# Optimization experiments

Hardware: AMD Instinct MI355X
Metric: run time of the kernel (lower is better)

Reference implementation:

```python
import jax, jax.numpy as jnp
import numpy as np

T, A, D = 1024, 512, 128
EPS = 1e-5
NEG_SLOPE = 0.01  # torch LeakyReLU default


def setup_inputs() -> dict:
    key = jax.random.key(0)
    ks = jax.random.split(key, 5)
    return {
        "nf_task": jax.random.normal(ks[0], (T, D), dtype=jnp.float32),
        "nf_agent": jax.random.normal(ks[1], (A, D), dtype=jnp.float32),
        "W1": jax.random.normal(ks[2], (D, 2 * D), dtype=jnp.float32) * 0.05,
        "gamma1": jnp.ones((D,), dtype=jnp.float32),
        "beta1": jnp.zeros((D,), dtype=jnp.float32),
        "W2": jax.random.normal(ks[3], (1, D), dtype=jnp.float32) * 0.05,
        "gamma2": jnp.ones((1,), dtype=jnp.float32),
        "beta2": jnp.zeros((1,), dtype=jnp.float32),
        "finished": jax.random.randint(ks[4], (T,), 0, 2, dtype=jnp.int32),
    }


def reference(nf_task, nf_agent, W1, gamma1, beta1, W2, gamma2, beta2, finished):
    d = nf_task.shape[1]
    # Linear(2D->D, no bias) on concat([src, dst]) == src @ W_src^T + dst @ W_dst^T
    src_proj = nf_task @ W1[:, :d].T   # [T, D]
    dst_proj = nf_agent @ W1[:, d:].T  # [A, D]
    h = src_proj[:, None, :] + dst_proj[None, :, :]  # per-edge hidden [T, A, D]
    # BatchNorm1d(D), training mode: batch stats over all edges
    mean = h.mean(axis=(0, 1))
    var = h.var(axis=(0, 1))  # biased, as torch uses for normalization
    h = (h - mean) * jax.lax.rsqrt(var + EPS) * gamma1 + beta1
    # LeakyReLU
    h = jnp.where(h >= 0, h, NEG_SLOPE * h)
    # Linear(D->1, no bias)
    s = jnp.einsum('tad,d->ta', h, W2[0])  # [T, A]
    # BatchNorm1d(1), training mode over all edges
    m2 = s.mean()
    v2 = s.var()
    s = (s - m2) * jax.lax.rsqrt(v2 + EPS) * gamma2[0] + beta2[0]
    # mask edges whose src task is finished
    s = jnp.where(finished.astype(bool)[:, None], -jnp.inf, s)
    # reduce: each agent's mailbox = scores over incoming tasks -> policy [A, T]
    return s.T
```

## Files before the change

### kernel.cpp

```cpp
#include <hip/hip_runtime.h>
#include <math.h>
#include <float.h>

#define T_N 1024
#define A_N 512
#define D_N 128
#define EPS 1e-5f
#define LDP 132

#define WS_SP   0
#define WS_DP   (WS_SP + T_N*D_N)
#define WS_SUMS (WS_DP + A_N*D_N)
#define WS_P    (WS_SUMS + 512)
#define WS_Q    (WS_P + T_N)
#define WS_S2   (WS_Q + A_N)
#define WS_ST   199168
#define N2F     ((float)(T_N * A_N))

__global__ __launch_bounds__(64) void k1_proj(const float* __restrict__ task,
                                              const float* __restrict__ agent,
                                              const float* __restrict__ W1,
                                              float* __restrict__ ws)
{
    __shared__ float RT[32 * LDP];
    __shared__ float WT[32 * LDP];
    int b = blockIdx.x;
    int rt = b >> 2, ct = b & 3;
    int tid = threadIdx.x;

    if (b == 0) {
        for (int i = 0; i < 8; i++) ws[WS_SUMS + tid + i * 64] = 0.f;
    }

    const float* src; float* dst; int woff, rbase;
    if (rt < 32) { src = task;  dst = ws + WS_SP; woff = 0;    rbase = rt * 32; }
    else         { src = agent; dst = ws + WS_DP; woff = D_N;  rbase = (rt - 32) * 32; }
    int cbase = ct * 32;

    {
        int rr = tid >> 5;
        int k  = (tid & 31) * 4;
        for (int it = 0; it < 16; it++) {
            int r = it * 2 + rr;
            *(float4*)(RT + r * LDP + k) = *(const float4*)(src + (rbase + r) * D_N + k);
        }
        for (int it = 0; it < 16; it++) {
            int j = it * 2 + rr;
            *(float4*)(WT + j * LDP + k) = *(const float4*)(W1 + (cbase + j) * (2 * D_N) + woff + k);
        }
    }
    __syncthreads();

    int rg = tid >> 3, cg = tid & 7;
    float acc[4][4] = {};
    for (int kk = 0; kk < 32; kk++) {
        float4 rv[4], wv[4];
        for (int i = 0; i < 4; i++) rv[i] = *(const float4*)(RT + (rg + 8 * i) * LDP + kk * 4);
        for (int j = 0; j < 4; j++) wv[j] = *(const float4*)(WT + (cg + 8 * j) * LDP + kk * 4);
        for (int i = 0; i < 4; i++)
            for (int j = 0; j < 4; j++)
                acc[i][j] += rv[i].x * wv[j].x + rv[i].y * wv[j].y
                           + rv[i].z * wv[j].z + rv[i].w * wv[j].w;
    }
    for (int i = 0; i < 4; i++)
        for (int j = 0; j < 4; j++)
            dst[(rbase + rg + 8 * i) * D_N + cbase + cg + 8 * j] = acc[i][j];
}

__global__ __launch_bounds__(256) void k2_stats(float* __restrict__ ws)
{
    int b = blockIdx.x, tid = threadIdx.x;
    int j = tid & 127, rh = tid >> 7;
    const float* src; float* sums; int rbase;
    if (b < 32) { src = ws + WS_SP; sums = ws + WS_SUMS;       rbase = b * 32; }
    else        { src = ws + WS_DP; sums = ws + WS_SUMS + 256; rbase = (b - 32) * 32; }
    float s = 0.f, q = 0.f;
    for (int i = 0; i < 16; i++) {
        float v = src[(rbase + i * 2 + rh) * D_N + j];
        s += v; q += v * v;
    }
    atomicAdd(&sums[j], s);
    atomicAdd(&sums[j + 128], q);
}

__global__ __launch_bounds__(64) void k2b_scale_pq(const float* __restrict__ g1,
                                                   const float* __restrict__ b1,
                                                   const float* __restrict__ W2,
                                                   float* __restrict__ ws)
{
    __shared__ float sc[128], sh[128], wl[128];
    int b = blockIdx.x, tid = threadIdx.x;
    if (b == 0 && tid < 2) ws[WS_S2 + tid] = 0.f;

    for (int h = 0; h < 2; h++) {
        int j = tid + 64 * h;
        float ms = ws[WS_SUMS + j]       * (1.f / T_N);
        float vs = ws[WS_SUMS + 128 + j] * (1.f / T_N) - ms * ms;
        float md = ws[WS_SUMS + 256 + j] * (1.f / A_N);
        float vd = ws[WS_SUMS + 384 + j] * (1.f / A_N) - md * md;
        float mean = ms + md, var = vs + vd;
        float s = g1[j] / sqrtf(var + EPS);
        sc[j] = s;
        sh[j] = b1[j] - mean * s;
        wl[j] = W2[j];
    }
    __syncthreads();

    float* rows; float* PQ; int rbase; bool isdp;
    if (b < 128) { rows = ws + WS_SP; PQ = ws + WS_P; rbase = b * 8;         isdp = false; }
    else         { rows = ws + WS_DP; PQ = ws + WS_Q; rbase = (b - 128) * 8; isdp = true;  }

    int l = tid;
    for (int r = 0; r < 8; r++) {
        int row = rbase + r;
        float v0 = rows[row * D_N + l];
        float v1 = rows[row * D_N + 64 + l];
        v0 = v0 * sc[l]      + (isdp ? sh[l]      : 0.f);
        v1 = v1 * sc[l + 64] + (isdp ? sh[l + 64] : 0.f);
        rows[row * D_N + l]      = v0;
        rows[row * D_N + 64 + l] = v1;
        float p = v0 * wl[l] + v1 * wl[l + 64];
        for (int off = 32; off >= 1; off >>= 1) p += __shfl_xor(p, off);
        if (l == 0) PQ[row] = 0.505f * p;
    }
}

#define TT 64
#define TA 32
__global__ __launch_bounds__(256) void kd_main(const float* __restrict__ W2,
                                               float* __restrict__ ws)
{
    __shared__ float spT[TT * LDP];
    __shared__ float dpT[TA * LDP];
    __shared__ float w495[128];
    __shared__ float Pl[TT], Ql[TA];
    __shared__ float stile[TA * 68];
    __shared__ float red[512];

    int tid = threadIdx.x;
    int rowbase = blockIdx.x * TT;
    int colbase = blockIdx.y * TA;

    {
        int k  = (tid & 31) * 4;
        int r8 = tid >> 5;
        for (int it = 0; it < 8; it++) {
            int t = it * 8 + r8;
            *(float4*)(spT + t * LDP + k) = *(const float4*)(ws + WS_SP + (rowbase + t) * D_N + k);
        }
        for (int it = 0; it < 4; it++) {
            int a = it * 8 + r8;
            *(float4*)(dpT + a * LDP + k) = *(const float4*)(ws + WS_DP + (colbase + a) * D_N + k);
        }
    }
    if (tid < 128) w495[tid] = 0.495f * W2[tid];
    if (tid < TT)  Pl[tid] = ws[WS_P + rowbase + tid];
    if (tid >= 128 && tid < 128 + TA) Ql[tid - 128] = ws[WS_Q + colbase + (tid - 128)];
    __syncthreads();

    int tx = tid & 15, ty = tid >> 4;
    float acc[4][2] = {};
    for (int kk = 0; kk < 32; kk++) {
        float4 wv = *(const float4*)(w495 + kk * 4);
        float4 sv[4], dv[2];
        for (int i = 0; i < 4; i++) sv[i] = *(const float4*)(spT + (ty + 16 * i) * LDP + kk * 4);
        for (int a = 0; a < 2; a++) dv[a] = *(const float4*)(dpT + (tx + 16 * a) * LDP + kk * 4);
        for (int i = 0; i < 4; i++)
            for (int a = 0; a < 2; a++) {
                float u;
                u = sv[i].x + dv[a].x; acc[i][a] += wv.x * fabsf(u);
                u = sv[i].y + dv[a].y; acc[i][a] += wv.y * fabsf(u);
                u = sv[i].z + dv[a].z; acc[i][a] += wv.z * fabsf(u);
                u = sv[i].w + dv[a].w; acc[i][a] += wv.w * fabsf(u);
            }
    }

    float lsum = 0.f, lsq = 0.f;
    for (int i = 0; i < 4; i++) {
        float p = Pl[ty + 16 * i];
        for (int a = 0; a < 2; a++) {
            float s = p + Ql[tx + 16 * a] + acc[i][a];
            lsum += s; lsq += s * s;
            stile[(tx + 16 * a) * 68 + ty + 16 * i] = s;
        }
    }
    red[tid] = lsum; red[256 + tid] = lsq;
    __syncthreads();
    for (int off = 128; off > 0; off >>= 1) {
        if (tid < off) { red[tid] += red[tid + off]; red[256 + tid] += red[256 + tid + off]; }
        __syncthreads();
    }
    if (tid == 0) {
        atomicAdd(ws + WS_S2,     red[0]);
        atomicAdd(ws + WS_S2 + 1, red[256]);
    }

    float* sT = ws + WS_ST;
    {
        int k4 = (tid & 15) * 4, row = tid >> 4;
        for (int it = 0; it < 2; it++) {
            int a = it * 16 + row;
            *(float4*)(sT + (colbase + a) * T_N + rowbase + k4) =
                *(const float4*)(stile + a * 68 + k4);
        }
    }
}

__global__ __launch_bounds__(256) void ke_final(const float* __restrict__ g2,
                                                const float* __restrict__ b2,
                                                const int* __restrict__ fin,
                                                const float* __restrict__ ws,
                                                float* __restrict__ out)
{
    float s2s = ws[WS_S2], s2q = ws[WS_S2 + 1];
    float m2 = s2s / N2F;
    float v2 = s2q / N2F - m2 * m2;
    float sc2 = g2[0] / sqrtf(v2 + EPS);
    float sh2 = b2[0] - m2 * sc2;
    const float NEG = -1.0e38f;

    int idx4 = blockIdx.x * 256 + threadIdx.x;
    int t4 = (idx4 & 255) * 4;
    float4 v = *((const float4*)(ws + WS_ST) + idx4);
    int4 f = *(const int4*)(fin + t4);
    float4 o;
    o.x = f.x ? NEG : v.x * sc2 + sh2;
    o.y = f.y ? NEG : v.y * sc2 + sh2;
    o.z = f.z ? NEG : v.z * sc2 + sh2;
    o.w = f.w ? NEG : v.w * sc2 + sh2;
    *((float4*)out + idx4) = o;
}

extern "C" void kernel_launch(void* const* d_in, const int* in_sizes, int n_in,
                              void* d_out, int out_size, void* d_ws, size_t ws_size,
                              hipStream_t stream) {
    (void)in_sizes; (void)n_in; (void)out_size; (void)ws_size;
    const float* task  = (const float*)d_in[0];
    const float* agent = (const float*)d_in[1];
    const float* W1    = (const float*)d_in[2];
    const float* g1    = (const float*)d_in[3];
    const float* b1    = (const float*)d_in[4];
    const float* W2    = (const float*)d_in[5];
    const float* g2    = (const float*)d_in[6];
    const float* b2    = (const float*)d_in[7];
    const int*   fin   = (const int*)d_in[8];
    float* out = (float*)d_out;
    float* ws  = (float*)d_ws;

    k1_proj<<<192, 64, 0, stream>>>(task, agent, W1, ws);
    k2_stats<<<48, 256, 0, stream>>>(ws);
    k2b_scale_pq<<<192, 64, 0, stream>>>(g1, b1, W2, ws);
    kd_main<<<dim3(16, 16), 256, 0, stream>>>(W2, ws);
    ke_final<<<512, 256, 0, stream>>>(g2, b2, fin, ws, out);
}
```

Before: 103.5 us.

## Fuse BN stats into projection and BN scaling into main kernel, drop atomics

Removes the separate stats and scale/PQ kernels. Column sums and sums of squares are now computed inside the projection epilogue as per-block partials, and the main kernel reduces those partials and applies the BN1 scale and shift while loading tiles. The LeakyReLU linear term is folded into the inner loop (0.505*w*u plus 0.495*w*|u|) instead of precomputed P/Q vectors, which adds an FMA per element in the hot loop. Global atomics are replaced by per-block partial writes reduced in the final kernel, and the final kernel processes two float4 per thread, cutting launches from five to three.

```diff
diff --git a/kernel.cpp b/kernel.cpp
--- a/kernel.cpp
+++ b/kernel.cpp
@@ -1,6 +1,5 @@
 #include <hip/hip_runtime.h>
 #include <math.h>
-#include <float.h>
 
 #define T_N 1024
 #define A_N 512
@@ -9,44 +8,46 @@
 #define LDP 132
 
 #define WS_SP   0
-#define WS_DP   (WS_SP + T_N*D_N)
-#define WS_SUMS (WS_DP + A_N*D_N)
-#define WS_P    (WS_SUMS + 512)
-#define WS_Q    (WS_P + T_N)
-#define WS_S2   (WS_Q + A_N)
-#define WS_ST   199168
+#define WS_DP   (T_N*D_N)
+#define WS_PS   (WS_DP + A_N*D_N)
+#define WS_SQ   (WS_PS + 48*128)
+#define WS_WC   (WS_SQ + 48*128)
+#define WS_S2P  (WS_WC + 256)
+#define WS_S2Q  (WS_S2P + 256)
+#define WS_ST   (WS_S2Q + 256)
 #define N2F     ((float)(T_N * A_N))
 
-__global__ __launch_bounds__(64) void k1_proj(const float* __restrict__ task,
+__global__ __launch_bounds__(64) void kp_proj(const float* __restrict__ task,
                                               const float* __restrict__ agent,
                                               const float* __restrict__ W1,
+                                              const float* __restrict__ W2,
                                               float* __restrict__ ws)
 {
     __shared__ float RT[32 * LDP];
     __shared__ float WT[32 * LDP];
-    int b = blockIdx.x;
+    int b = blockIdx.x, tid = threadIdx.x;
     int rt = b >> 2, ct = b & 3;
-    int tid = threadIdx.x;
 
     if (b == 0) {
-        for (int i = 0; i < 8; i++) ws[WS_SUMS + tid + i * 64] = 0.f;
+        for (int h = 0; h < 2; h++) {
+            int j = tid + 64 * h;
+            float w = W2[j];
+            ws[WS_WC + j]       = 0.505f * w;
+            ws[WS_WC + 128 + j] = 0.495f * w;
+        }
     }
 
     const float* src; float* dst; int woff, rbase;
-    if (rt < 32) { src = task;  dst = ws + WS_SP; woff = 0;    rbase = rt * 32; }
-    else         { src = agent; dst = ws + WS_DP; woff = D_N;  rbase = (rt - 32) * 32; }
+    if (rt < 32) { src = task;  dst = ws + WS_SP; woff = 0;   rbase = rt * 32; }
+    else         { src = agent; dst = ws + WS_DP; woff = D_N; rbase = (rt - 32) * 32; }
     int cbase = ct * 32;
 
     {
-        int rr = tid >> 5;
-        int k  = (tid & 31) * 4;
+        int rr = tid >> 5, k = (tid & 31) * 4;
         for (int it = 0; it < 16; it++) {
             int r = it * 2 + rr;
             *(float4*)(RT + r * LDP + k) = *(const float4*)(src + (rbase + r) * D_N + k);
-        }
-        for (int it = 0; it < 16; it++) {
-            int j = it * 2 + rr;
-            *(float4*)(WT + j * LDP + k) = *(const float4*)(W1 + (cbase + j) * (2 * D_N) + woff + k);
+            *(float4*)(WT + r * LDP + k) = *(const float4*)(W1 + (cbase + r) * (2 * D_N) + woff + k);
         }
     }
     __syncthreads();
@@ -62,142 +63,129 @@
                 acc[i][j] += rv[i].x * wv[j].x + rv[i].y * wv[j].y
                            + rv[i].z * wv[j].z + rv[i].w * wv[j].w;
     }
+
     for (int i = 0; i < 4; i++)
         for (int j = 0; j < 4; j++)
             dst[(rbase + rg + 8 * i) * D_N + cbase + cg + 8 * j] = acc[i][j];
-}
-
-__global__ __launch_bounds__(256) void k2_stats(float* __restrict__ ws)
-{
-    int b = blockIdx.x, tid = threadIdx.x;
-    int j = tid & 127, rh = tid >> 7;
-    const float* src; float* sums; int rbase;
-    if (b < 32) { src = ws + WS_SP; sums = ws + WS_SUMS;       rbase = b * 32; }
-    else        { src = ws + WS_DP; sums = ws + WS_SUMS + 256; rbase = (b - 32) * 32; }
-    float s = 0.f, q = 0.f;
-    for (int i = 0; i < 16; i++) {
-        float v = src[(rbase + i * 2 + rh) * D_N + j];
-        s += v; q += v * v;
-    }
-    atomicAdd(&sums[j], s);
-    atomicAdd(&sums[j + 128], q);
-}
-
-__global__ __launch_bounds__(64) void k2b_scale_pq(const float* __restrict__ g1,
-                                                   const float* __restrict__ b1,
-                                                   const float* __restrict__ W2,
-                                                   float* __restrict__ ws)
-{
-    __shared__ float sc[128], sh[128], wl[128];
-    int b = blockIdx.x, tid = threadIdx.x;
-    if (b == 0 && tid < 2) ws[WS_S2 + tid] = 0.f;
-
-    for (int h = 0; h < 2; h++) {
-        int j = tid + 64 * h;
-        float ms = ws[WS_SUMS + j]       * (1.f / T_N);
-        float vs = ws[WS_SUMS + 128 + j] * (1.f / T_N) - ms * ms;
-        float md = ws[WS_SUMS + 256 + j] * (1.f / A_N);
-        float vd = ws[WS_SUMS + 384 + j] * (1.f / A_N) - md * md;
-        float mean = ms + md, var = vs + vd;
-        float s = g1[j] / sqrtf(var + EPS);
-        sc[j] = s;
-        sh[j] = b1[j] - mean * s;
-        wl[j] = W2[j];
-    }
-    __syncthreads();
-
-    float* rows; float* PQ; int rbase; bool isdp;
-    if (b < 128) { rows = ws + WS_SP; PQ = ws + WS_P; rbase = b * 8;         isdp = false; }
-    else         { rows = ws + WS_DP; PQ = ws + WS_Q; rbase = (b - 128) * 8; isdp = true;  }
-
-    int l = tid;
-    for (int r = 0; r < 8; r++) {
-        int row = rbase + r;
-        float v0 = rows[row * D_N + l];
-        float v1 = rows[row * D_N + 64 + l];
-        v0 = v0 * sc[l]      + (isdp ? sh[l]      : 0.f);
-        v1 = v1 * sc[l + 64] + (isdp ? sh[l + 64] : 0.f);
-        rows[row * D_N + l]      = v0;
-        rows[row * D_N + 64 + l] = v1;
-        float p = v0 * wl[l] + v1 * wl[l + 64];
-        for (int off = 32; off >= 1; off >>= 1) p += __shfl_xor(p, off);
-        if (l == 0) PQ[row] = 0.505f * p;
-    }
+
+    float csum[4], csq[4];
+    for (int j = 0; j < 4; j++) {
+        csum[j] = acc[0][j] + acc[1][j] + acc[2][j] + acc[3][j];
+        csq[j]  = acc[0][j]*acc[0][j] + acc[1][j]*acc[1][j]
+                + acc[2][j]*acc[2][j] + acc[3][j]*acc[3][j];
+    }
+    for (int off = 8; off <= 32; off <<= 1)
+        for (int j = 0; j < 4; j++) {
+            csum[j] += __shfl_xor(csum[j], off);
+            csq[j]  += __shfl_xor(csq[j],  off);
+        }
+    if (tid < 8)
+        for (int j = 0; j < 4; j++) {
+            ws[WS_PS + rt * 128 + cbase + tid + 8 * j] = csum[j];
+            ws[WS_SQ + rt * 128 + cbase + tid + 8 * j] = csq[j];
+        }
 }
 
 #define TT 64
 #define TA 32
-__global__ __launch_bounds__(256) void kd_main(const float* __restrict__ W2,
+__global__ __launch_bounds__(256) void kd_main(const float* __restrict__ g1,
+                                               const float* __restrict__ b1,
                                                float* __restrict__ ws)
 {
     __shared__ float spT[TT * LDP];
     __shared__ float dpT[TA * LDP];
-    __shared__ float w495[128];
-    __shared__ float Pl[TT], Ql[TA];
+    __shared__ float scs[128], shs[128];
     __shared__ float stile[TA * 68];
     __shared__ float red[512];
 
     int tid = threadIdx.x;
-    int rowbase = blockIdx.x * TT;
-    int colbase = blockIdx.y * TA;
+    int rowbase = blockIdx.x * TT, colbase = blockIdx.y * TA;
+
+    if (tid < 128) {
+        float as = 0.f, ds = 0.f;
+        for (int r = 0;  r < 32; r++) as += ws[WS_PS + r * 128 + tid];
+        for (int r = 32; r < 48; r++) ds += ws[WS_PS + r * 128 + tid];
+        red[tid] = as; red[128 + tid] = ds;
+    } else {
+        int j = tid - 128;
+        float aq = 0.f, dq = 0.f;
+        for (int r = 0;  r < 32; r++) aq += ws[WS_SQ + r * 128 + j];
+        for (int r = 32; r < 48; r++) dq += ws[WS_SQ + r * 128 + j];
+        red[256 + j] = aq; red[384 + j] = dq;
+    }
+    __syncthreads();
+    if (tid < 128) {
+        float ms = red[tid] * (1.f / T_N);
+        float md = red[128 + tid] * (1.f / A_N);
+        float var = red[256 + tid] * (1.f / T_N) - ms * ms
+                  + red[384 + tid] * (1.f / A_N) - md * md;
+        float s = g1[tid] * rsqrtf(var + EPS);
+        scs[tid] = s;
+        shs[tid] = b1[tid] - (ms + md) * s;
+    }
+    __syncthreads();
 
     {
-        int k  = (tid & 31) * 4;
-        int r8 = tid >> 5;
+        int k = (tid & 31) * 4, r8 = tid >> 5;
+        float4 sc4 = *(const float4*)(scs + k);
+        float4 sh4 = *(const float4*)(shs + k);
         for (int it = 0; it < 8; it++) {
             int t = it * 8 + r8;
-            *(float4*)(spT + t * LDP + k) = *(const float4*)(ws + WS_SP + (rowbase + t) * D_N + k);
+            float4 v = *(const float4*)(ws + WS_SP + (rowbase + t) * D_N + k);
+            v.x *= sc4.x; v.y *= sc4.y; v.z *= sc4.z; v.w *= sc4.w;
+            *(float4*)(spT + t * LDP + k) = v;
         }
         for (int it = 0; it < 4; it++) {
             int a = it * 8 + r8;
-            *(float4*)(dpT + a * LDP + k) = *(const float4*)(ws + WS_DP + (colbase + a) * D_N + k);
-        }
-    }
-    if (tid < 128) w495[tid] = 0.495f * W2[tid];
-    if (tid < TT)  Pl[tid] = ws[WS_P + rowbase + tid];
-    if (tid >= 128 && tid < 128 + TA) Ql[tid - 128] = ws[WS_Q + colbase + (tid - 128)];
+            float4 v = *(const float4*)(ws + WS_DP + (colbase + a) * D_N + k);
+            v.x = v.x * sc4.x + sh4.x; v.y = v.y * sc4.y + sh4.y;
+            v.z = v.z * sc4.z + sh4.z; v.w = v.w * sc4.w + sh4.w;
+            *(float4*)(dpT + a * LDP + k) = v;
+        }
+    }
     __syncthreads();
 
     int tx = tid & 15, ty = tid >> 4;
+    const float* w5p = ws + WS_WC;
+    const float* w9p = ws + WS_WC + 128;
     float acc[4][2] = {};
     for (int kk = 0; kk < 32; kk++) {
-        float4 wv = *(const float4*)(w495 + kk * 4);
+        float4 w5 = *(const float4*)(w5p + kk * 4);
+        float4 w9 = *(const float4*)(w9p + kk * 4);
         float4 sv[4], dv[2];
         for (int i = 0; i < 4; i++) sv[i] = *(const float4*)(spT + (ty + 16 * i) * LDP + kk * 4);
         for (int a = 0; a < 2; a++) dv[a] = *(const float4*)(dpT + (tx + 16 * a) * LDP + kk * 4);
         for (int i = 0; i < 4; i++)
             for (int a = 0; a < 2; a++) {
                 float u;
-                u = sv[i].x + dv[a].x; acc[i][a] += wv.x * fabsf(u);
-                u = sv[i].y + dv[a].y; acc[i][a] += wv.y * fabsf(u);
-                u = sv[i].z + dv[a].z; acc[i][a] += wv.z * fabsf(u);
-                u = sv[i].w + dv[a].w; acc[i][a] += wv.w * fabsf(u);
+                u = sv[i].x + dv[a].x; acc[i][a] += w5.x * u + w9.x * fabsf(u);
+                u = sv[i].y + dv[a].y; acc[i][a] += w5.y * u + w9.y * fabsf(u);
+                u = sv[i].z + dv[a].z; acc[i][a] += w5.z * u + w9.z * fabsf(u);
+                u = sv[i].w + dv[a].w; acc[i][a] += w5.w * u + w9.w * fabsf(u);
             }
     }
 
     float lsum = 0.f, lsq = 0.f;
-    for (int i = 0; i < 4; i++) {
-        float p = Pl[ty + 16 * i];
+    for (int i = 0; i < 4; i++)
         for (int a = 0; a < 2; a++) {
-            float s = p + Ql[tx + 16 * a] + acc[i][a];
+            float s = acc[i][a];
             lsum += s; lsq += s * s;
             stile[(tx + 16 * a) * 68 + ty + 16 * i] = s;
         }
-    }
-    red[tid] = lsum; red[256 + tid] = lsq;
-    __syncthreads();
-    for (int off = 128; off > 0; off >>= 1) {
-        if (tid < off) { red[tid] += red[tid + off]; red[256 + tid] += red[256 + tid + off]; }
-        __syncthreads();
-    }
+    for (int off = 1; off <= 32; off <<= 1) {
+        lsum += __shfl_xor(lsum, off);
+        lsq  += __shfl_xor(lsq,  off);
+    }
+    int wid = tid >> 6;
+    if ((tid & 63) == 0) { red[wid] = lsum; red[8 + wid] = lsq; }
+    __syncthreads();
     if (tid == 0) {
-        atomicAdd(ws + WS_S2,     red[0]);
-        atomicAdd(ws + WS_S2 + 1, red[256]);
-    }
-
-    float* sT = ws + WS_ST;
+        ws[WS_S2P + blockIdx.y * 16 + blockIdx.x] = red[0] + red[1] + red[2] + red[3];
+        ws[WS_S2Q + blockIdx.y * 16 + blockIdx.x] = red[8] + red[9] + red[10] + red[11];
+    }
     {
         int k4 = (tid & 15) * 4, row = tid >> 4;
+        float* sT = ws + WS_ST;
         for (int it = 0; it < 2; it++) {
             int a = it * 16 + row;
             *(float4*)(sT + (colbase + a) * T_N + rowbase + k4) =
@@ -212,23 +200,36 @@
                                                 const float* __restrict__ ws,
                                                 float* __restrict__ out)
 {
-    float s2s = ws[WS_S2], s2q = ws[WS_S2 + 1];
-    float m2 = s2s / N2F;
-    float v2 = s2q / N2F - m2 * m2;
-    float sc2 = g2[0] / sqrtf(v2 + EPS);
+    __shared__ float r2[16];
+    int tid = threadIdx.x;
+    float v1 = ws[WS_S2P + tid];
+    float v2 = ws[WS_S2Q + tid];
+    for (int off = 1; off <= 32; off <<= 1) {
+        v1 += __shfl_xor(v1, off);
+        v2 += __shfl_xor(v2, off);
+    }
+    if ((tid & 63) == 0) { r2[tid >> 6] = v1; r2[8 + (tid >> 6)] = v2; }
+    __syncthreads();
+    float s2s = r2[0] + r2[1] + r2[2] + r2[3];
+    float s2q = r2[8] + r2[9] + r2[10] + r2[11];
+    float m2  = s2s / N2F;
+    float var2 = s2q / N2F - m2 * m2;
+    float sc2 = g2[0] * rsqrtf(var2 + EPS);
     float sh2 = b2[0] - m2 * sc2;
     const float NEG = -1.0e38f;
 
-    int idx4 = blockIdx.x * 256 + threadIdx.x;
-    int t4 = (idx4 & 255) * 4;
-    float4 v = *((const float4*)(ws + WS_ST) + idx4);
-    int4 f = *(const int4*)(fin + t4);
-    float4 o;
-    o.x = f.x ? NEG : v.x * sc2 + sh2;
-    o.y = f.y ? NEG : v.y * sc2 + sh2;
-    o.z = f.z ? NEG : v.z * sc2 + sh2;
-    o.w = f.w ? NEG : v.w * sc2 + sh2;
-    *((float4*)out + idx4) = o;
+    for (int h = 0; h < 2; h++) {
+        int idx4 = blockIdx.x * 256 + tid + h * 65536;
+        int t4 = (idx4 & 255) * 4;
+        float4 v = *((const float4*)(ws + WS_ST) + idx4);
+        int4 f = *(const int4*)(fin + t4);
+        float4 o;
+        o.x = f.x ? NEG : v.x * sc2 + sh2;
+        o.y = f.y ? NEG : v.y * sc2 + sh2;
+        o.z = f.z ? NEG : v.z * sc2 + sh2;
+        o.w = f.w ? NEG : v.w * sc2 + sh2;
+        *((float4*)out + idx4) = o;
+    }
 }
 
 extern "C" void kernel_launch(void* const* d_in, const int* in_sizes, int n_in,
@@ -247,9 +248,7 @@
     float* out = (float*)d_out;
     float* ws  = (float*)d_ws;
 
-    k1_proj<<<192, 64, 0, stream>>>(task, agent, W1, ws);
-    k2_stats<<<48, 256, 0, stream>>>(ws);
-    k2b_scale_pq<<<192, 64, 0, stream>>>(g1, b1, W2, ws);
-    kd_main<<<dim3(16, 16), 256, 0, stream>>>(W2, ws);
-    ke_final<<<512, 256, 0, stream>>>(g2, b2, fin, ws, out);
-}
+    kp_proj<<<192, 64, 0, stream>>>(task, agent, W1, W2, ws);
+    kd_main<<<dim3(16, 16), 256, 0, stream>>>(g1, b1, ws);
+    ke_final<<<256, 256, 0, stream>>>(g2, b2, fin, ws, out);
+}
```

Result: faster. 93.27 us (-9.9%).
